# Kernel tuning notes

Measured on AMD Instinct MI355X. Metric: run time of the kernel, lower is better.

## Reference

```python
import jax, jax.numpy as jnp
import numpy as np


def setup_inputs() -> dict:
    key = jax.random.key(0)
    k1, k2, k3, k4 = jax.random.split(key, 4)
    B, T_dec, T_enc, H2 = 8, 64, 512, 512  # H2 = 2*hiddenSize
    encoderOutput = jax.random.normal(k1, (B, T_enc, H2), dtype=jnp.float32)
    decoderInput = jax.random.normal(k2, (B, T_dec, H2), dtype=jnp.float32)
    # fc: Linear(4H -> 2H); torch weight layout [out, in] = [2H, 4H]
    W = jax.random.normal(k3, (H2, 2 * H2), dtype=jnp.float32) * (1.0 / np.sqrt(2 * H2))
    b = jax.random.normal(k4, (H2,), dtype=jnp.float32) * 0.01
    return {"encoderOutput": encoderOutput, "decoderInput": decoderInput, "W": W, "b": b}


def reference(encoderOutput, decoderInput, W, b):
    # Original: for each (i, j), fc(cat(dec[:,i], enc[:,j])) then log_softmax over
    # the FEATURE dim (dim=1 of the flattened [-1, 2H] tensor), then
    # context[:, i] = sum_j log_softmax(...) * enc[:, j].
    H2 = encoderOutput.shape[-1]
    W_dec = W[:, :H2]   # columns multiplying the decoder half of the concat
    W_enc = W[:, H2:]   # columns multiplying the encoder half
    dec_part = jnp.einsum('bid,od->bio', decoderInput, W_dec)   # [B, T_dec, 2H]
    enc_part = jnp.einsum('bjd,od->bjo', encoderOutput, W_enc)  # [B, T_enc, 2H]
    logits = dec_part[:, :, None, :] + enc_part[:, None, :, :] + b  # [B, T_dec, T_enc, 2H]
    alpha = jax.nn.log_softmax(logits, axis=-1)  # softmax over feature dim, as in source
    context = jnp.einsum('bijd,bjd->bid', alpha, encoderOutput)  # [B, T_dec, 2H]
    return context
```

## Files before the change

kernel.cpp:

```cpp
#include <hip/hip_runtime.h>


namespace {
constexpr int kH  = 512;
constexpr int kTD = 64;
constexpr int kTE = 512;
constexpr int kB  = 8;
constexpr int kRD = kB * kTD;
constexpr int kRE = kB * kTE;
}

typedef __attribute__((ext_vector_type(8))) short short8;
typedef __attribute__((ext_vector_type(4))) float floatx4;

__device__ __forceinline__ unsigned short f2bf(float x) {
    unsigned u = __float_as_uint(x);
    u += 0x7fffu + ((u >> 16) & 1u);
    return (unsigned short)(u >> 16);
}
__device__ __forceinline__ float bf2f(unsigned short h) {
    return __uint_as_float(((unsigned)h) << 16);
}
__device__ __forceinline__ size_t fragTile(int rtile, int kt) {
    return ((size_t)rtile * 16 + kt) * 512;
}
__device__ __forceinline__ short8 pack8(float4 a, float4 b) {
    short8 r;
    r[0] = (short)f2bf(a.x); r[1] = (short)f2bf(a.y);
    r[2] = (short)f2bf(a.z); r[3] = (short)f2bf(a.w);
    r[4] = (short)f2bf(b.x); r[5] = (short)f2bf(b.y);
    r[6] = (short)f2bf(b.z); r[7] = (short)f2bf(b.w);
    return r;
}

__global__ __launch_bounds__(256) void fused_cast(
    const float* __restrict__ W, const float* __restrict__ dec,
    const float* __restrict__ enc,
    unsigned short* __restrict__ Wd_f, unsigned short* __restrict__ We_f,
    unsigned short* __restrict__ dec_f,
    unsigned short* __restrict__ enc_f, unsigned short* __restrict__ encT_f,
    float* __restrict__ S12)
{
    const int blk = blockIdx.x, t = threadIdx.x;
    const int w = t >> 6, l = t & 63;
    const int lr = l & 15, lc = l >> 4;
    if (blk < 256) {
        const int gw = blk * 4 + w;
        const int sel = gw >> 9, rem = gw & 511;
        const int ot = rem >> 4, kt = rem & 15;
        const int o = ot * 16 + lr;
        const float* src = W + (size_t)o * 1024 + sel * 512 + kt * 32 + lc * 8;
        const float4 v0 = *(const float4*)src;
        const float4 v1 = *(const float4*)(src + 4);
        unsigned short* dst = (sel ? We_f : Wd_f) + fragTile(ot, kt) + l * 8;
        *(short8*)dst = pack8(v0, v1);
        if (blk < 32) S12[blk * 256 + t] = 0.f;
    } else if (blk < 384) {
        const int gw = (blk - 256) * 4 + w;
        const int rt = gw >> 4, kt = gw & 15;
        const int r = rt * 16 + lr;
        const float* src = dec + (size_t)r * kH + kt * 32 + lc * 8;
        const float4 v0 = *(const float4*)src;
        const float4 v1 = *(const float4*)(src + 4);
        *(short8*)(dec_f + fragTile(rt, kt) + l * 8) = pack8(v0, v1);
    } else {
        __shared__ unsigned short s[64][36];
        const int e = blk - 384;
        const int kt = e & 15, jt = (e >> 4) & 7, b = e >> 7;
        const int j0 = jt * 64, d0 = kt * 32;
        const int jl = w * 16 + lr;
        const float* src = enc + ((size_t)(b * kTE + j0 + jl)) * kH + d0 + lc * 8;
        const float4 v0 = *(const float4*)src;
        const float4 v1 = *(const float4*)(src + 4);
        const short8 p = pack8(v0, v1);
        *(short8*)(enc_f + fragTile(b * 32 + jt * 4 + w, kt) + l * 8) = p;
#pragma unroll
        for (int i = 0; i < 8; ++i) s[jl][lc * 8 + i] = (unsigned short)p[i];
        __syncthreads();
        const int dt = w >> 1, jc = w & 1;
        const int dl = dt * 16 + lr;
        const int j8 = jc * 32 + lc * 8;
        short8 v;
#pragma unroll
        for (int i = 0; i < 8; ++i) v[i] = (short)s[j8 + i][dl];
        *(short8*)(encT_f + fragTile(b * 32 + kt * 2 + dt, jt * 2 + jc) + l * 8) = v;
    }
}

__global__ __launch_bounds__(256) void gemm1(
    const unsigned short* __restrict__ enc_f,
    const unsigned short* __restrict__ dec_f,
    const unsigned short* __restrict__ Wd_f,
    const unsigned short* __restrict__ We_f,
    const float* __restrict__ bias,
    unsigned short* __restrict__ part_bf, unsigned short* __restrict__ uv_f)
{
    __shared__ float As[64][68];
    const int tile = blockIdx.x;
    const int ns = tile & 7, ms = tile >> 3;
    const int t = threadIdx.x, w = t >> 6, l = t & 63;
    const int qm = w >> 1, qn = w & 1;
    const bool isenc = (ms >= 8);
    const unsigned short* A = isenc ? enc_f : dec_f;
    const unsigned short* Bw = isenc ? We_f : Wd_f;
    const int art = (isenc ? (ms - 8) : ms) * 4 + qm * 2;
    const int brt = ns * 4 + qn * 2;

    floatx4 acc[2][2];
#pragma unroll
    for (int m = 0; m < 2; ++m)
#pragma unroll
        for (int n = 0; n < 2; ++n) acc[m][n] = (floatx4){0.f, 0.f, 0.f, 0.f};

    for (int kt = 0; kt < 16; ++kt) {
        short8 af[2], bfr[2];
#pragma unroll
        for (int m = 0; m < 2; ++m)
            af[m] = *(const short8*)(A + fragTile(art + m, kt) + l * 8);
#pragma unroll
        for (int n = 0; n < 2; ++n)
            bfr[n] = *(const short8*)(Bw + fragTile(brt + n, kt) + l * 8);
#pragma unroll
        for (int m = 0; m < 2; ++m)
#pragma unroll
            for (int n = 0; n < 2; ++n)
                acc[m][n] = __builtin_amdgcn_mfma_f32_16x16x32_bf16(af[m], bfr[n], acc[m][n], 0, 0, 0);
    }

    const int lr = l & 15, lq = l >> 4;
#pragma unroll
    for (int m = 0; m < 2; ++m)
#pragma unroll
        for (int n = 0; n < 2; ++n)
#pragma unroll
            for (int r = 0; r < 4; ++r)
                As[qm * 32 + m * 16 + lq * 4 + r][qn * 32 + n * 16 + lr] = acc[m][n][r];
    __syncthreads();

    const int rowbase = ms * 64, colbase = ns * 64;
#pragma unroll
    for (int h = 0; h < 2; ++h) {
        const int a = h * 256 + t;
        const int row = a >> 3, cc = (a & 7) * 8;
        const float4 v0 = *(const float4*)&As[row][cc];
        const float4 v1 = *(const float4*)&As[row][cc + 4];
        *(short8*)(part_bf + (size_t)(rowbase + row) * kH + colbase + cc) = pack8(v0, v1);
    }
#pragma unroll
    for (int h = 0; h < 2; ++h) {
        const int s = h * 256 + t;
        const int rt = s >> 7, kc = (s >> 6) & 1, fl = s & 63;
        const int row = rt * 16 + (fl & 15);
        const int col = kc * 32 + (fl >> 4) * 8;
        const float4 v0 = *(const float4*)&As[row][col];
        const float4 v1 = *(const float4*)&As[row][col + 4];
        float4 b0 = make_float4(0.f, 0.f, 0.f, 0.f), b1 = b0;
        if (isenc) {
            b0 = *(const float4*)(bias + colbase + col);
            b1 = *(const float4*)(bias + colbase + col + 4);
        }
        short8 u;
        u[0] = (short)f2bf(__expf(v0.x + b0.x));
        u[1] = (short)f2bf(__expf(v0.y + b0.y));
        u[2] = (short)f2bf(__expf(v0.z + b0.z));
        u[3] = (short)f2bf(__expf(v0.w + b0.w));
        u[4] = (short)f2bf(__expf(v1.x + b1.x));
        u[5] = (short)f2bf(__expf(v1.y + b1.y));
        u[6] = (short)f2bf(__expf(v1.z + b1.z));
        u[7] = (short)f2bf(__expf(v1.w + b1.w));
        *(short8*)(uv_f + fragTile(ms * 4 + rt, ns * 2 + kc) + fl * 8) = u;
    }
}

__global__ __launch_bounds__(256) void lse_s1s2(
    const unsigned short* __restrict__ uv_f, unsigned short* __restrict__ lse_f,
    const float* __restrict__ enc, const unsigned short* __restrict__ part_bf,
    float* __restrict__ S12)
{
    __shared__ float red[4][16][68];
    const int blk = blockIdx.x, t = threadIdx.x;
    if (blk < 256) {
        const int b = blk >> 5, rem = blk & 31;
        const int it = rem >> 3, jt = rem & 7;
        const int w = t >> 6, l = t & 63;
        const int art = b * 4 + it;
        const int vrt0 = 32 + b * 32 + jt * 4;

        floatx4 acc[4];
#pragma unroll
        for (int n = 0; n < 4; ++n) acc[n] = (floatx4){0.f, 0.f, 0.f, 0.f};
#pragma unroll
        for (int kk = 0; kk < 4; ++kk) {
            const int kt = w * 4 + kk;
            const short8 af = *(const short8*)(uv_f + fragTile(art, kt) + l * 8);
#pragma unroll
            for (int n = 0; n < 4; ++n)
                acc[n] = __builtin_amdgcn_mfma_f32_16x16x32_bf16(
                    af, *(const short8*)(uv_f + fragTile(vrt0 + n, kt) + l * 8), acc[n], 0, 0, 0);
        }
        const int lr = l & 15, lq = l >> 4;
#pragma unroll
        for (int n = 0; n < 4; ++n)
#pragma unroll
            for (int r = 0; r < 4; ++r)
                red[w][lq * 4 + r][n * 16 + lr] = acc[n][r];
        __syncthreads();
        const int s = t >> 1, h = t & 1;
        const int kc = s >> 6, fl = s & 63;
        const int i = fl & 15;
        const int j = kc * 32 + (fl >> 4) * 8 + h * 4;
        float4 sum = *(const float4*)&red[0][i][j];
        const float4 s1 = *(const float4*)&red[1][i][j];
        const float4 s2 = *(const float4*)&red[2][i][j];
        const float4 s3 = *(const float4*)&red[3][i][j];
        sum.x += s1.x + s2.x + s3.x; sum.y += s1.y + s2.y + s3.y;
        sum.z += s1.z + s2.z + s3.z; sum.w += s1.w + s2.w + s3.w;
        ushort4 o;
        o.x = f2bf(__logf(sum.x)); o.y = f2bf(__logf(sum.y));
        o.z = f2bf(__logf(sum.z)); o.w = f2bf(__logf(sum.w));
        *(ushort4*)(lse_f + fragTile(b * 4 + it, jt * 2 + kc) + fl * 8 + h * 4) = o;
    } else {
        const int blk2 = blk - 256;
        const int jc = blk2 & 15, b = (blk2 >> 4) & 7, dh = blk2 >> 7;
        const int d = dh * 256 + t;
        const float* e = enc + ((size_t)b * kTE + jc * 32) * kH + d;
        const unsigned short* p = part_bf + (size_t)(kRD + b * kTE + jc * 32) * kH + d;
        float s1 = 0.f, s2 = 0.f;
#pragma unroll 4
        for (int j = 0; j < 32; ++j) {
            const float ev = e[(size_t)j * kH];
            const float pv = bf2f(p[(size_t)j * kH]);
            s1 += ev;
            s2 = fmaf(pv, ev, s2);
        }
        atomicAdd(&S12[b * kH + d], s1);
        atomicAdd(&S12[4096 + b * kH + d], s2);
    }
}

__global__ __launch_bounds__(256) void final_k(
    const unsigned short* __restrict__ lse_f,
    const unsigned short* __restrict__ encT_f,
    const unsigned short* __restrict__ part_bf,
    const float* __restrict__ bias,
    const float* __restrict__ S12,
    float* __restrict__ out)
{
    __shared__ float red[4][16][68];
    const int blk = blockIdx.x, t = threadIdx.x;
    const int b = blk >> 5, rem = blk & 31;
    const int it = rem >> 3, dt = rem & 7;
    const int w = t >> 6, l = t & 63;
    const int art = b * 4 + it;
    const int brt0 = b * 32 + dt * 4;

    floatx4 acc[4];
#pragma unroll
    for (int n = 0; n < 4; ++n) acc[n] = (floatx4){0.f, 0.f, 0.f, 0.f};
#pragma unroll
    for (int kk = 0; kk < 4; ++kk) {
        const int kt = w * 4 + kk;
        const short8 af = *(const short8*)(lse_f + fragTile(art, kt) + l * 8);
#pragma unroll
        for (int n = 0; n < 4; ++n)
            acc[n] = __builtin_amdgcn_mfma_f32_16x16x32_bf16(
                af, *(const short8*)(encT_f + fragTile(brt0 + n, kt) + l * 8), acc[n], 0, 0, 0);
    }
    const int lr = l & 15, lq = l >> 4;
#pragma unroll
    for (int n = 0; n < 4; ++n)
#pragma unroll
        for (int r = 0; r < 4; ++r)
            red[w][lq * 4 + r][n * 16 + lr] = acc[n][r];
    __syncthreads();
    const int i = t >> 4, d0 = (t & 15) * 4;
    float4 m = *(const float4*)&red[0][i][d0];
    const float4 m1 = *(const float4*)&red[1][i][d0];
    const float4 m2 = *(const float4*)&red[2][i][d0];
    const float4 m3 = *(const float4*)&red[3][i][d0];
    m.x += m1.x + m2.x + m3.x; m.y += m1.y + m2.y + m3.y;
    m.z += m1.z + m2.z + m3.z; m.w += m1.w + m2.w + m3.w;

    const int gd = dt * 64 + d0;
    const float4 s1 = *(const float4*)(S12 + b * kH + gd);
    const float4 s2 = *(const float4*)(S12 + 4096 + b * kH + gd);
    const float4 bi = *(const float4*)(bias + gd);
    const int row = b * kTD + it * 16 + i;
    const ushort4 dp = *(const ushort4*)(part_bf + (size_t)row * kH + gd);
    float4 o;
    o.x = fmaf(bf2f(dp.x) + bi.x, s1.x, s2.x) - m.x;
    o.y = fmaf(bf2f(dp.y) + bi.y, s1.y, s2.y) - m.y;
    o.z = fmaf(bf2f(dp.z) + bi.z, s1.z, s2.z) - m.z;
    o.w = fmaf(bf2f(dp.w) + bi.w, s1.w, s2.w) - m.w;
    *(float4*)(out + (size_t)row * kH + gd) = o;
}

extern "C" void kernel_launch(void* const* d_in, const int* in_sizes, int n_in,
                              void* d_out, int out_size, void* d_ws, size_t ws_size,
                              hipStream_t stream)
{
    (void)in_sizes; (void)n_in; (void)out_size; (void)ws_size;
    const float* enc  = (const float*)d_in[0];
    const float* dec  = (const float*)d_in[1];
    const float* W    = (const float*)d_in[2];
    const float* bias = (const float*)d_in[3];
    float* out = (float*)d_out;

    char* base = (char*)d_ws;
    unsigned short* part_bf = (unsigned short*)(base);
    unsigned short* uv_f    = (unsigned short*)(base + 4718592);
    unsigned short* enc_f   = (unsigned short*)(base + 9437184);
    unsigned short* encT_f  = (unsigned short*)(base + 13631488);
    unsigned short* dec_f   = (unsigned short*)(base + 17825792);
    unsigned short* Wd_f    = (unsigned short*)(base + 18350080);
    unsigned short* We_f    = (unsigned short*)(base + 18874368);
    unsigned short* lse_f   = (unsigned short*)(base + 19398656);
    float*          S12     = (float*)(base + 19922944);

    fused_cast<<<1408, 256, 0, stream>>>(W, dec, enc, Wd_f, We_f, dec_f,
                                         enc_f, encT_f, S12);
    gemm1<<<576, 256, 0, stream>>>(enc_f, dec_f, Wd_f, We_f, bias, part_bf, uv_f);
    lse_s1s2<<<512, 256, 0, stream>>>(uv_f, lse_f, enc, part_bf, S12);
    final_k<<<256, 256, 0, stream>>>(lse_f, encT_f, part_bf, bias, S12, out);
}
```

Baseline: 91.26 us.

## Fuse S1/S2 encoder reductions into gemm1 epilogue and drop encoder part store

Encoder tiles of gemm1 now compute the column sums of enc and of part*enc directly from the fp32 accumulator tile in shared memory. They reduce within the block before issuing atomics. This removes the bf16 store of the encoder projection and its reread in a separate kernel branch, leaving a smaller lse-only kernel. It adds extra shared memory and a global read of enc to gemm1's epilogue, which may lower occupancy.

Measured after the change: 91.87 us. No clear change (+0.7%).

```diff
diff --git a/kernel.cpp b/kernel.cpp
--- a/kernel.cpp
+++ b/kernel.cpp
@@ -93,9 +93,13 @@
     const unsigned short* __restrict__ Wd_f,
     const unsigned short* __restrict__ We_f,
     const float* __restrict__ bias,
-    unsigned short* __restrict__ part_bf, unsigned short* __restrict__ uv_f)
+    const float* __restrict__ enc,
+    unsigned short* __restrict__ part_bf, unsigned short* __restrict__ uv_f,
+    float* __restrict__ S12)
 {
     __shared__ float As[64][68];
+    __shared__ float r1[16][68];
+    __shared__ float r2[16][68];
     const int tile = blockIdx.x;
     const int ns = tile & 7, ms = tile >> 3;
     const int t = threadIdx.x, w = t >> 6, l = t & 63;
@@ -138,13 +142,15 @@
     __syncthreads();
 
     const int rowbase = ms * 64, colbase = ns * 64;
-#pragma unroll
-    for (int h = 0; h < 2; ++h) {
-        const int a = h * 256 + t;
-        const int row = a >> 3, cc = (a & 7) * 8;
-        const float4 v0 = *(const float4*)&As[row][cc];
-        const float4 v1 = *(const float4*)&As[row][cc + 4];
-        *(short8*)(part_bf + (size_t)(rowbase + row) * kH + colbase + cc) = pack8(v0, v1);
+    if (!isenc) {
+#pragma unroll
+        for (int h = 0; h < 2; ++h) {
+            const int a = h * 256 + t;
+            const int row = a >> 3, cc = (a & 7) * 8;
+            const float4 v0 = *(const float4*)&As[row][cc];
+            const float4 v1 = *(const float4*)&As[row][cc + 4];
+            *(short8*)(part_bf + (size_t)(rowbase + row) * kH + colbase + cc) = pack8(v0, v1);
+        }
     }
 #pragma unroll
     for (int h = 0; h < 2; ++h) {
@@ -170,72 +176,81 @@
         u[7] = (short)f2bf(__expf(v1.w + b1.w));
         *(short8*)(uv_f + fragTile(ms * 4 + rt, ns * 2 + kc) + fl * 8) = u;
     }
-}
-
-__global__ __launch_bounds__(256) void lse_s1s2(
-    const unsigned short* __restrict__ uv_f, unsigned short* __restrict__ lse_f,
-    const float* __restrict__ enc, const unsigned short* __restrict__ part_bf,
-    float* __restrict__ S12)
+    if (isenc) {
+        const int b = (ms - 8) >> 3;
+        const int jbase = ((ms - 8) & 7) * 64;
+        const int o4 = (t & 15) * 4, jg = t >> 4;
+        float4 s1p = make_float4(0.f, 0.f, 0.f, 0.f);
+        float4 s2p = make_float4(0.f, 0.f, 0.f, 0.f);
+#pragma unroll
+        for (int jj = 0; jj < 4; ++jj) {
+            const int j = jg * 4 + jj;
+            const float4 ev = *(const float4*)(
+                enc + ((size_t)(b * kTE + jbase + j)) * kH + colbase + o4);
+            const float4 pv = *(const float4*)&As[j][o4];
+            s1p.x += ev.x; s1p.y += ev.y; s1p.z += ev.z; s1p.w += ev.w;
+            s2p.x = fmaf(pv.x, ev.x, s2p.x);
+            s2p.y = fmaf(pv.y, ev.y, s2p.y);
+            s2p.z = fmaf(pv.z, ev.z, s2p.z);
+            s2p.w = fmaf(pv.w, ev.w, s2p.w);
+        }
+        *(float4*)&r1[jg][o4] = s1p;
+        *(float4*)&r2[jg][o4] = s2p;
+        __syncthreads();
+        if (t < 64) {
+            float a1 = 0.f, a2 = 0.f;
+#pragma unroll
+            for (int g = 0; g < 16; ++g) { a1 += r1[g][t]; a2 += r2[g][t]; }
+            atomicAdd(&S12[b * kH + colbase + t], a1);
+            atomicAdd(&S12[4096 + b * kH + colbase + t], a2);
+        }
+    }
+}
+
+__global__ __launch_bounds__(256) void lse_k(
+    const unsigned short* __restrict__ uv_f, unsigned short* __restrict__ lse_f)
 {
     __shared__ float red[4][16][68];
     const int blk = blockIdx.x, t = threadIdx.x;
-    if (blk < 256) {
-        const int b = blk >> 5, rem = blk & 31;
-        const int it = rem >> 3, jt = rem & 7;
-        const int w = t >> 6, l = t & 63;
-        const int art = b * 4 + it;
-        const int vrt0 = 32 + b * 32 + jt * 4;
-
-        floatx4 acc[4];
-#pragma unroll
-        for (int n = 0; n < 4; ++n) acc[n] = (floatx4){0.f, 0.f, 0.f, 0.f};
-#pragma unroll
-        for (int kk = 0; kk < 4; ++kk) {
-            const int kt = w * 4 + kk;
-            const short8 af = *(const short8*)(uv_f + fragTile(art, kt) + l * 8);
-#pragma unroll
-            for (int n = 0; n < 4; ++n)
-                acc[n] = __builtin_amdgcn_mfma_f32_16x16x32_bf16(
-                    af, *(const short8*)(uv_f + fragTile(vrt0 + n, kt) + l * 8), acc[n], 0, 0, 0);
-        }
-        const int lr = l & 15, lq = l >> 4;
+    const int b = blk >> 5, rem = blk & 31;
+    const int it = rem >> 3, jt = rem & 7;
+    const int w = t >> 6, l = t & 63;
+    const int art = b * 4 + it;
+    const int vrt0 = 32 + b * 32 + jt * 4;
+
+    floatx4 acc[4];
+#pragma unroll
+    for (int n = 0; n < 4; ++n) acc[n] = (floatx4){0.f, 0.f, 0.f, 0.f};
+#pragma unroll
+    for (int kk = 0; kk < 4; ++kk) {
+        const int kt = w * 4 + kk;
+        const short8 af = *(const short8*)(uv_f + fragTile(art, kt) + l * 8);
 #pragma unroll
         for (int n = 0; n < 4; ++n)
-#pragma unroll
-            for (int r = 0; r < 4; ++r)
-                red[w][lq * 4 + r][n * 16 + lr] = acc[n][r];
-        __syncthreads();
-        const int s = t >> 1, h = t & 1;
-        const int kc = s >> 6, fl = s & 63;
-        const int i = fl & 15;
-        const int j = kc * 32 + (fl >> 4) * 8 + h * 4;
-        float4 sum = *(const float4*)&red[0][i][j];
-        const float4 s1 = *(const float4*)&red[1][i][j];
-        const float4 s2 = *(const float4*)&red[2][i][j];
-        const float4 s3 = *(const float4*)&red[3][i][j];
-        sum.x += s1.x + s2.x + s3.x; sum.y += s1.y + s2.y + s3.y;
-        sum.z += s1.z + s2.z + s3.z; sum.w += s1.w + s2.w + s3.w;
-        ushort4 o;
-        o.x = f2bf(__logf(sum.x)); o.y = f2bf(__logf(sum.y));
-        o.z = f2bf(__logf(sum.z)); o.w = f2bf(__logf(sum.w));
-        *(ushort4*)(lse_f + fragTile(b * 4 + it, jt * 2 + kc) + fl * 8 + h * 4) = o;
-    } else {
-        const int blk2 = blk - 256;
-        const int jc = blk2 & 15, b = (blk2 >> 4) & 7, dh = blk2 >> 7;
-        const int d = dh * 256 + t;
-        const float* e = enc + ((size_t)b * kTE + jc * 32) * kH + d;
-        const unsigned short* p = part_bf + (size_t)(kRD + b * kTE + jc * 32) * kH + d;
-        float s1 = 0.f, s2 = 0.f;
-#pragma unroll 4
-        for (int j = 0; j < 32; ++j) {
-            const float ev = e[(size_t)j * kH];
-            const float pv = bf2f(p[(size_t)j * kH]);
-            s1 += ev;
-            s2 = fmaf(pv, ev, s2);
-        }
-        atomicAdd(&S12[b * kH + d], s1);
-        atomicAdd(&S12[4096 + b * kH + d], s2);
-    }
+            acc[n] = __builtin_amdgcn_mfma_f32_16x16x32_bf16(
+                af, *(const short8*)(uv_f + fragTile(vrt0 + n, kt) + l * 8), acc[n], 0, 0, 0);
+    }
+    const int lr = l & 15, lq = l >> 4;
+#pragma unroll
+    for (int n = 0; n < 4; ++n)
+#pragma unroll
+        for (int r = 0; r < 4; ++r)
+            red[w][lq * 4 + r][n * 16 + lr] = acc[n][r];
+    __syncthreads();
+    const int s = t >> 1, h = t & 1;
+    const int kc = s >> 6, fl = s & 63;
+    const int i = fl & 15;
+    const int j = kc * 32 + (fl >> 4) * 8 + h * 4;
+    float4 sum = *(const float4*)&red[0][i][j];
+    const float4 s1 = *(const float4*)&red[1][i][j];
+    const float4 s2 = *(const float4*)&red[2][i][j];
+    const float4 s3 = *(const float4*)&red[3][i][j];
+    sum.x += s1.x + s2.x + s3.x; sum.y += s1.y + s2.y + s3.y;
+    sum.z += s1.z + s2.z + s3.z; sum.w += s1.w + s2.w + s3.w;
+    ushort4 o;
+    o.x = f2bf(__logf(sum.x)); o.y = f2bf(__logf(sum.y));
+    o.z = f2bf(__logf(sum.z)); o.w = f2bf(__logf(sum.w));
+    *(ushort4*)(lse_f + fragTile(b * 4 + it, jt * 2 + kc) + fl * 8 + h * 4) = o;
 }
 
 __global__ __launch_bounds__(256) void final_k(
@@ -319,7 +334,8 @@
 
     fused_cast<<<1408, 256, 0, stream>>>(W, dec, enc, Wd_f, We_f, dec_f,
                                          enc_f, encT_f, S12);
-    gemm1<<<576, 256, 0, stream>>>(enc_f, dec_f, Wd_f, We_f, bias, part_bf, uv_f);
-    lse_s1s2<<<512, 256, 0, stream>>>(uv_f, lse_f, enc, part_bf, S12);
+    gemm1<<<576, 256, 0, stream>>>(enc_f, dec_f, Wd_f, We_f, bias, enc,
+                                   part_bf, uv_f, S12);
+    lse_k<<<256, 256, 0, stream>>>(uv_f, lse_f);
     final_k<<<256, 256, 0, stream>>>(lse_f, encT_f, part_bf, bias, S12, out);
 }
```
